# Performance work log

Hardware: AMD Instinct MI355X
Metric: run time of the kernel (lower is better)

## Reference

```python
import jax, jax.numpy as jnp
import numpy as np


def _pool_mat(N, pn):
    # F.interpolate(mode='area') == adaptive_avg_pool1d: output i averages
    # input indices [floor(i*N/pn), ceil((i+1)*N/pn))
    W = np.zeros((pn, N), dtype=np.float32)
    for i in range(pn):
        s = (i * N) // pn
        e = -((-(i + 1) * N) // pn)  # ceil((i+1)*N/pn)
        W[i, s:e] = 1.0 / (e - s)
    return W


def _up_mat(pn, N):
    # F.interpolate(mode='linear', align_corners=False) from length pn to N
    W = np.zeros((N, pn), dtype=np.float32)
    scale = pn / N
    for j in range(N):
        pos = max((j + 0.5) * scale - 0.5, 0.0)
        i0 = min(int(np.floor(pos)), pn - 1)
        i1 = min(i0 + 1, pn - 1)
        frac = pos - i0
        W[j, i0] += 1.0 - frac
        W[j, i1] += frac
    return W


def setup_inputs() -> dict:
    key = jax.random.key(0)
    k1, k2 = jax.random.split(key)
    B, N, C, K = 512, 16, 256, 8192
    f = jax.random.normal(k1, (B, N, C), dtype=jnp.float32)
    # original init: uniform(-1/K, 1/K)
    emb = jax.random.uniform(k2, (K, C), dtype=jnp.float32, minval=-1.0 / K, maxval=1.0 / K)
    return {"f": f, "emb": emb}


def reference(f, emb):
    B, N, C = f.shape
    fT = jnp.transpose(f, (0, 2, 1))            # [B, C, N]
    f_ng = jax.lax.stop_gradient(fT)
    emb_ng = jax.lax.stop_gradient(emb)
    e_sq = jnp.sum(emb_ng * emb_ng, axis=1)     # [K]
    f_rest = f_ng
    f_hat = jnp.zeros_like(f_ng)
    commit = jnp.float32(0.0)
    qlat = jnp.float32(0.0)
    for pn in range(1, N + 1):
        rest_bcn = jax.lax.stop_gradient(f_rest)
        if pn < N:
            Wp = jnp.asarray(_pool_mat(N, pn))             # [pn, N]
            rest = jnp.einsum('pn,bcn->bpc', Wp, rest_bcn).reshape(-1, C)
        else:
            rest = jnp.transpose(rest_bcn, (0, 2, 1)).reshape(-1, C)
        # squared euclidean distances [B*pn, K]
        d = jnp.sum(rest * rest, axis=1, keepdims=True) + e_sq - 2.0 * (rest @ emb_ng.T)
        idx = jnp.argmin(d, axis=1).reshape(B, pn)
        h = jnp.transpose(emb[idx], (0, 2, 1))             # [B, C, pn]
        if pn < N:
            Wu = jnp.asarray(_up_mat(pn, N))               # [N, pn]
            h = jnp.einsum('np,bcp->bcn', Wu, h)
        f_hat = f_hat + h
        f_rest = f_rest - h
        commit = commit + 0.25 * jnp.mean((jax.lax.stop_gradient(f_hat) - fT) ** 2)
        qlat = qlat + jnp.mean((f_hat - f_ng) ** 2)
    commit = commit / N
    qlat = qlat / N
    # straight-through estimator
    f_hat_out = jax.lax.stop_gradient(f_hat) - f_ng + fT
    return jnp.transpose(f_hat_out, (0, 2, 1)), commit, qlat
```

## Files before the change

### kernel.cpp

```cpp
#include <hip/hip_runtime.h>
#include <math.h>

#define BB 512
#define NN 16
#define CC 256
#define KK 8192
#define BNC (BB*NN*CC)

typedef unsigned short u16;
typedef __attribute__((ext_vector_type(8))) short bf16x8;
typedef __attribute__((ext_vector_type(4))) float f32x4;

__device__ __forceinline__ u16 f2bf(float x) {
    unsigned u = __float_as_uint(x);
    unsigned r = (u + 0x7fffu + ((u >> 16) & 1u)) >> 16;
    return (u16)r;
}

__device__ __forceinline__ void gl2lds16(const void* g, void* l) {
    __builtin_amdgcn_global_load_lds(
        (const __attribute__((address_space(1))) void*)g,
        (__attribute__((address_space(3))) void*)l,
        16, 0, 0);
}

__device__ __forceinline__ void gl2lds4(const void* g, void* l) {
    __builtin_amdgcn_global_load_lds(
        (const __attribute__((address_space(1))) void*)g,
        (__attribute__((address_space(3))) void*)l,
        4, 0, 0);
}

__global__ void esq_kernel(const float* __restrict__ emb, float* __restrict__ e_sq) {
    int gid  = blockIdx.x * blockDim.x + threadIdx.x;
    int wave = gid >> 6;
    int lane = gid & 63;
    const float4 v = *(const float4*)(emb + (size_t)wave * CC + lane * 4);
    float s = v.x*v.x + v.y*v.y + v.z*v.z + v.w*v.w;
    #pragma unroll
    for (int m = 32; m >= 1; m >>= 1) s += __shfl_xor(s, m, 64);
    if (lane == 0) e_sq[wave] = 0.5f * s;
}

__global__ void cvt_emb_kernel(const float* __restrict__ emb, u16* __restrict__ out) {
    int gid = blockIdx.x * blockDim.x + threadIdx.x;
    float4 v = ((const float4*)emb)[gid];
    ushort4 o;
    o.x = f2bf(-v.x); o.y = f2bf(-v.y); o.z = f2bf(-v.z); o.w = f2bf(-v.w);
    ((ushort4*)out)[gid] = o;
}

__global__ void init_pool_kernel(const float* __restrict__ f,
                                 u16* __restrict__ rest_bf) {
    int b = blockIdx.x;
    int c = threadIdx.x;
    const float* base = f + (size_t)b * NN * CC + c;
    float acc = 0.f;
    #pragma unroll
    for (int n = 0; n < NN; ++n) acc += base[(size_t)n * CC];
    rest_bf[(size_t)b * CC + c] = f2bf(acc * (1.0f / 16.0f));
}

__device__ __forceinline__ unsigned long long shfl_xor_u64(unsigned long long v, int m) {
    unsigned lo = (unsigned)v, hi = (unsigned)(v >> 32);
    lo = __shfl_xor(lo, m, 64);
    hi = __shfl_xor(hi, m, 64);
    return ((unsigned long long)hi << 32) | lo;
}

__global__ __launch_bounds__(256, 2) void dist_mfma_kernel(
        const u16* __restrict__ A, const u16* __restrict__ Bm,
        const float* __restrict__ e_sq,
        unsigned long long* __restrict__ packed, int cpb) {
    __shared__ __align__(16) u16 sC[32768];
    __shared__ __align__(16) float sE[512];
    const int tid = threadIdx.x;
    const int w = tid >> 6, l = tid & 63;
    const int r0 = blockIdx.x * 64;
    const int c0 = blockIdx.y * cpb;
    const int ncb = cpb >> 8;
    const int tmax = ncb * 8 - 1;
    const int arow = l & 15;
    const int aq   = l >> 4;

    bf16x8 bf[4][8];
    {
        const u16* fb = A + (((size_t)(r0 + arow)) << 8) + aq * 8;
        #pragma unroll
        for (int j = 0; j < 4; ++j)
            #pragma unroll
            for (int kc = 0; kc < 8; ++kc)
                bf[j][kc] = *(const bf16x8*)(fb + (j << 12) + (kc << 5));
    }

    const int loff = ((l >> 2) << 8) + ((l & 3) << 3);
    const u16* Pb = Bm + (((size_t)(c0 + w * 64)) << 8) + loff;
    char* ldsc = (char*)sC + (w << 14);
    const float* ebuf = sE + (w << 7);

    #define STAGEC(t_, buf_) { \
        const int tt_ = ((t_) > tmax) ? tmax : (t_); \
        const u16* s_ = Pb + (((size_t)(tt_ >> 3)) << 16) + ((tt_ & 7) << 5); \
        char* d_ = ldsc + ((buf_) << 12); \
        gl2lds16(s_,          d_); \
        gl2lds16(s_ + 4096,   d_ + 1024); \
        gl2lds16(s_ + 8192,   d_ + 2048); \
        gl2lds16(s_ + 12288,  d_ + 3072); }

    #define STAGEE(cb_) { \
        const int cc_ = ((cb_) >= ncb) ? (ncb - 1) : (cb_); \
        gl2lds4(e_sq + c0 + cc_ * 256 + w * 64 + l, \
                (char*)sE + ((((w << 1) | ((cb_) & 1))) << 8)); }

    STAGEE(0)
    STAGEC(0, 0) STAGEC(1, 1) STAGEC(2, 2)

    float bestd[4];
    int   bestk[4];
    #pragma unroll
    for (int j = 0; j < 4; ++j) { bestd[j] = 1e30f; bestk[j] = 0; }

    for (int cb = 0; cb < ncb; ++cb) {
        f32x4 acc[4][4];
        const int tb = cb * 8;
        #pragma unroll
        for (int kc = 0; kc < 8; ++kc) {
            if (kc >= 1 && kc <= 3) {
                asm volatile("s_waitcnt vmcnt(9)" ::: "memory");
            } else {
                asm volatile("s_waitcnt vmcnt(8)" ::: "memory");
            }
            if (kc == 0) {
                f32x4 eqv[4];
                #pragma unroll
                for (int i = 0; i < 4; ++i)
                    eqv[i] = *(const f32x4*)(ebuf + ((cb & 1) << 6) + i * 16 + (aq << 2));
                #pragma unroll
                for (int i = 0; i < 4; ++i)
                    #pragma unroll
                    for (int j = 0; j < 4; ++j) acc[i][j] = eqv[i];
            }
            const int t = tb + kc;
            bf16x8 cf[4];
            const u16* cbp = (const u16*)(ldsc + ((t & 3) << 12));
            #pragma unroll
            for (int i = 0; i < 4; ++i)
                cf[i] = *(const bf16x8*)(cbp + ((i * 16 + arow) << 5) + (aq << 3));
            STAGEC(t + 3, (t + 3) & 3)
            if (kc == 0) STAGEE(cb + 1)
            #pragma unroll
            for (int i = 0; i < 4; ++i)
                #pragma unroll
                for (int j = 0; j < 4; ++j)
                    acc[i][j] = __builtin_amdgcn_mfma_f32_16x16x32_bf16(
                                    cf[i], bf[j][kc], acc[i][j], 0, 0, 0);
        }

        #pragma unroll
        for (int i = 0; i < 4; ++i)
            #pragma unroll
            for (int r = 0; r < 4; ++r) {
                const int k = c0 + cb * 256 + w * 64 + i * 16 + (aq << 2) + r;
                #pragma unroll
                for (int j = 0; j < 4; ++j) {
                    const float d = acc[i][j][r];
                    if (d < bestd[j]) { bestd[j] = d; bestk[j] = k; }
                }
            }
    }
    #undef STAGEC
    #undef STAGEE

    #pragma unroll
    for (int j = 0; j < 4; ++j) {
        unsigned u = __float_as_uint(bestd[j]);
        u = (u & 0x80000000u) ? ~u : (u | 0x80000000u);
        unsigned long long p = ((unsigned long long)u << 32) | (unsigned)bestk[j];
        unsigned long long o = shfl_xor_u64(p, 16);
        if (o < p) p = o;
        o = shfl_xor_u64(p, 32);
        if (o < p) p = o;
        if (aq == 0)
            atomicMin(&packed[r0 + j * 16 + arow], p);
    }
}

__global__ void update_pool_kernel(const float* __restrict__ f,
                                   const float* __restrict__ emb,
                                   const unsigned long long* __restrict__ packed,
                                   float* __restrict__ f_rest,
                                   float* __restrict__ f_hat,
                                   float* __restrict__ slots,
                                   u16* __restrict__ rest_bf, int pn) {
    int b = blockIdx.x;
    int c = threadIdx.x;
    __shared__ int sk[NN];
    __shared__ float red[4];
    if (threadIdx.x < pn)
        sk[threadIdx.x] = (int)(unsigned)(packed[b * pn + threadIdx.x] & 0xffffffffull);
    __syncthreads();

    float fr[NN];
    float acc_sq = 0.f;
    #pragma unroll
    for (int n = 0; n < NN; ++n) {
        double pos = (n + 0.5) * ((double)pn / 16.0) - 0.5;
        if (pos < 0.0) pos = 0.0;
        int i0 = (int)floor(pos);
        if (i0 > pn - 1) i0 = pn - 1;
        int i1 = i0 + 1;
        if (i1 > pn - 1) i1 = pn - 1;
        double frac = pos - (double)i0;
        float w1 = (float)frac;
        float w0 = (float)(1.0 - frac);
        float h = w0 * emb[(size_t)sk[i0] * CC + c] + w1 * emb[(size_t)sk[i1] * CC + c];
        size_t off = ((size_t)b * NN + n) * CC + c;
        float fh = f_hat[off] + h;
        f_hat[off] = fh;
        float fre = f_rest[off] - h;
        f_rest[off] = fre;
        fr[n] = fre;
        float diff = fh - f[off];
        acc_sq += diff * diff;
    }

    int wv = threadIdx.x >> 6, ln = threadIdx.x & 63;
    #pragma unroll
    for (int m = 32; m >= 1; m >>= 1) acc_sq += __shfl_xor(acc_sq, m, 64);
    if (ln == 0) red[wv] = acc_sq;

    int pn2 = pn + 1;
    if (pn < NN) {
        for (int p = 0; p < pn2; ++p) {
            int s = (p * NN) / pn2;
            int e = ((p + 1) * NN + pn2 - 1) / pn2;
            float v = 0.f;
            for (int n = s; n < e; ++n) v += fr[n];
            v *= 1.0f / (float)(e - s);
            rest_bf[((size_t)(b * pn2 + p)) * CC + c] = f2bf(v);
        }
    }
    __syncthreads();
    if (threadIdx.x == 0)
        atomicAdd(&slots[b & 255], (red[0] + red[1]) + (red[2] + red[3]));
}

__global__ void final_kernel(const float* __restrict__ slots, float* __restrict__ out_scalars) {
    float v = slots[threadIdx.x];
    #pragma unroll
    for (int m = 32; m >= 1; m >>= 1) v += __shfl_xor(v, m, 64);
    __shared__ float red[4];
    int wv = threadIdx.x >> 6, ln = threadIdx.x & 63;
    if (ln == 0) red[wv] = v;
    __syncthreads();
    if (threadIdx.x == 0) {
        float S = (red[0] + red[1]) + (red[2] + red[3]);
        float qlat = S / (float)BNC / (float)NN;
        out_scalars[0] = 0.25f * qlat;
        out_scalars[1] = qlat;
    }
}

extern "C" void kernel_launch(void* const* d_in, const int* in_sizes, int n_in,
                              void* d_out, int out_size, void* d_ws, size_t ws_size,
                              hipStream_t stream) {
    (void)in_sizes; (void)n_in; (void)out_size; (void)ws_size;
    const float* f   = (const float*)d_in[0];
    const float* emb = (const float*)d_in[1];
    float* out = (float*)d_out;

    float* ws      = (float*)d_ws;
    float* f_rest  = ws;
    float* r2_pad  = f_rest + BNC;
    float* e_sq    = r2_pad + BB * NN;
    float* slots   = e_sq + KK;
    unsigned long long* packed_all = (unsigned long long*)(slots + 256);
    u16* rest_bf = (u16*)(packed_all + (size_t)BB * 136);
    u16* emb_bf  = rest_bf + (size_t)BB * NN * CC;

    float* f_hat = out;

    hipMemsetAsync(out, 0, (size_t)BNC * sizeof(float), stream);
    hipMemcpyAsync(f_rest, f, (size_t)BNC * sizeof(float), hipMemcpyDeviceToDevice, stream);
    hipMemsetAsync(slots, 0, 256 * sizeof(float), stream);
    hipMemsetAsync(packed_all, 0xFF, (size_t)BB * 136 * sizeof(unsigned long long), stream);
    esq_kernel<<<KK / 4, 256, 0, stream>>>(emb, e_sq);
    cvt_emb_kernel<<<KK * CC / 4 / 256, 256, 0, stream>>>(emb, emb_bf);
    init_pool_kernel<<<BB, 256, 0, stream>>>(f, rest_bf);

    static const int splits_tab[17] = {0,32,32,16,16,8,8,8,8,4,4,4,4,4,4,4,4};

    for (int pn = 1; pn <= NN; ++pn) {
        unsigned long long* packed = packed_all + (size_t)BB * (pn * (pn - 1) / 2);
        int splits = splits_tab[pn];
        int cpb = KK / splits;
        dim3 grid(BB * pn / 64, splits);
        dist_mfma_kernel<<<grid, 256, 0, stream>>>(rest_bf, emb_bf, e_sq, packed, cpb);
        update_pool_kernel<<<BB, 256, 0, stream>>>(f, emb, packed, f_rest, f_hat,
                                                   slots, rest_bf, pn);
    }
    final_kernel<<<1, 256, 0, stream>>>(slots, out + BNC);
}
```

Before: 772.0 us.

## Share codebook tiles across waves with 64-row-per-wave blocking in distance kernel

Restructures the distance MFMA kernel so each block covers 256 rows (64 per wave) and all waves share one codebook tile staged into LDS per step, instead of each wave streaming its own codebook slice. This cuts per-block global/LDS codebook traffic relative to compute. It adds an XOR swizzle to avoid LDS bank conflicts, preloads all e_sq values, and raises wave priority around MFMAs. It requires a workgroup barrier every k-step and retunes the K-split table to keep enough blocks.

Result: slower. 787.9 us (+2.1%).

```diff
diff --git a/kernel.cpp b/kernel.cpp
--- a/kernel.cpp
+++ b/kernel.cpp
@@ -76,16 +76,16 @@
     __shared__ __align__(16) float sE[512];
     const int tid = threadIdx.x;
     const int w = tid >> 6, l = tid & 63;
-    const int r0 = blockIdx.x * 64;
+    const int r0 = blockIdx.x * 256;
     const int c0 = blockIdx.y * cpb;
-    const int ncb = cpb >> 8;
-    const int tmax = ncb * 8 - 1;
+    const int nch = cpb >> 3;
+    const int ncb2 = cpb >> 6;
     const int arow = l & 15;
     const int aq   = l >> 4;
 
     bf16x8 bf[4][8];
     {
-        const u16* fb = A + (((size_t)(r0 + arow)) << 8) + aq * 8;
+        const u16* fb = A + (((size_t)(r0 + w * 64 + arow)) << 8) + aq * 8;
         #pragma unroll
         for (int j = 0; j < 4; ++j)
             #pragma unroll
@@ -93,74 +93,63 @@
                 bf[j][kc] = *(const bf16x8*)(fb + (j << 12) + (kc << 5));
     }
 
-    const int loff = ((l >> 2) << 8) + ((l & 3) << 3);
-    const u16* Pb = Bm + (((size_t)(c0 + w * 64)) << 8) + loff;
-    char* ldsc = (char*)sC + (w << 14);
-    const float* ebuf = sE + (w << 7);
-
-    #define STAGEC(t_, buf_) { \
-        const int tt_ = ((t_) > tmax) ? tmax : (t_); \
-        const u16* s_ = Pb + (((size_t)(tt_ >> 3)) << 16) + ((tt_ & 7) << 5); \
-        char* d_ = ldsc + ((buf_) << 12); \
-        gl2lds16(s_,          d_); \
-        gl2lds16(s_ + 4096,   d_ + 1024); \
-        gl2lds16(s_ + 8192,   d_ + 2048); \
-        gl2lds16(s_ + 12288,  d_ + 3072); }
-
-    #define STAGEE(cb_) { \
-        const int cc_ = ((cb_) >= ncb) ? (ncb - 1) : (cb_); \
-        gl2lds4(e_sq + c0 + cc_ * 256 + w * 64 + l, \
-                (char*)sE + ((((w << 1) | ((cb_) & 1))) << 8)); }
-
-    STAGEE(0)
-    STAGEC(0, 0) STAGEC(1, 1) STAGEC(2, 2)
-
+    for (int n = tid; n < cpb; n += 256)
+        gl2lds4(e_sq + c0 + n, (char*)sE + (size_t)(n - l) * 4);
+
+    const int crel = w * 16 + (l >> 2);
+    const int g = (l & 3) ^ ((l >> 3) & 3);
+    const u16* Pb = Bm + (((size_t)(c0 + crel)) << 8) + g * 8;
+
+    #define STAGEC(t_) { \
+        int tt_ = (t_); if (tt_ >= nch) tt_ = nch - 1; \
+        const u16* s_ = Pb + (((size_t)(tt_ >> 3)) << 14) + ((tt_ & 7) << 5); \
+        gl2lds16(s_, (char*)sC + (((t_) & 3) << 12) + (w << 10)); }
+
+    STAGEC(0) STAGEC(1) STAGEC(2)
+
+    const int gx = aq ^ ((arow >> 1) & 3);
     float bestd[4];
     int   bestk[4];
     #pragma unroll
     for (int j = 0; j < 4; ++j) { bestd[j] = 1e30f; bestk[j] = 0; }
 
-    for (int cb = 0; cb < ncb; ++cb) {
+    for (int cb = 0; cb < ncb2; ++cb) {
         f32x4 acc[4][4];
-        const int tb = cb * 8;
         #pragma unroll
         for (int kc = 0; kc < 8; ++kc) {
-            if (kc >= 1 && kc <= 3) {
-                asm volatile("s_waitcnt vmcnt(9)" ::: "memory");
-            } else {
-                asm volatile("s_waitcnt vmcnt(8)" ::: "memory");
+            const int t = cb * 8 + kc;
+            asm volatile("s_waitcnt vmcnt(2)" ::: "memory");
+            __builtin_amdgcn_s_barrier();
+            STAGEC(t + 3)
+            if (kc == 0) {
+                #pragma unroll
+                for (int i = 0; i < 4; ++i) {
+                    f32x4 ev = *(const f32x4*)(sE + cb * 64 + i * 16 + (aq << 2));
+                    #pragma unroll
+                    for (int j = 0; j < 4; ++j) acc[i][j] = ev;
+                }
             }
-            if (kc == 0) {
-                f32x4 eqv[4];
-                #pragma unroll
-                for (int i = 0; i < 4; ++i)
-                    eqv[i] = *(const f32x4*)(ebuf + ((cb & 1) << 6) + i * 16 + (aq << 2));
-                #pragma unroll
-                for (int i = 0; i < 4; ++i)
-                    #pragma unroll
-                    for (int j = 0; j < 4; ++j) acc[i][j] = eqv[i];
-            }
-            const int t = tb + kc;
             bf16x8 cf[4];
-            const u16* cbp = (const u16*)(ldsc + ((t & 3) << 12));
+            const u16* cbp = sC + ((t & 3) << 11);
             #pragma unroll
             for (int i = 0; i < 4; ++i)
-                cf[i] = *(const bf16x8*)(cbp + ((i * 16 + arow) << 5) + (aq << 3));
-            STAGEC(t + 3, (t + 3) & 3)
-            if (kc == 0) STAGEE(cb + 1)
+                cf[i] = *(const bf16x8*)(cbp + ((i * 16 + arow) << 5) + (gx << 3));
+            __builtin_amdgcn_s_setprio(1);
             #pragma unroll
             for (int i = 0; i < 4; ++i)
                 #pragma unroll
                 for (int j = 0; j < 4; ++j)
                     acc[i][j] = __builtin_amdgcn_mfma_f32_16x16x32_bf16(
                                     cf[i], bf[j][kc], acc[i][j], 0, 0, 0);
+            __builtin_amdgcn_s_setprio(0);
+            asm volatile("s_waitcnt lgkmcnt(0)" ::: "memory");
         }
 
         #pragma unroll
         for (int i = 0; i < 4; ++i)
             #pragma unroll
             for (int r = 0; r < 4; ++r) {
-                const int k = c0 + cb * 256 + w * 64 + i * 16 + (aq << 2) + r;
+                const int k = c0 + cb * 64 + i * 16 + (aq << 2) + r;
                 #pragma unroll
                 for (int j = 0; j < 4; ++j) {
                     const float d = acc[i][j][r];
@@ -169,7 +158,6 @@
             }
     }
     #undef STAGEC
-    #undef STAGEE
 
     #pragma unroll
     for (int j = 0; j < 4; ++j) {
@@ -181,7 +169,7 @@
         o = shfl_xor_u64(p, 32);
         if (o < p) p = o;
         if (aq == 0)
-            atomicMin(&packed[r0 + j * 16 + arow], p);
+            atomicMin(&packed[r0 + w * 64 + j * 16 + arow], p);
     }
 }
 
@@ -288,13 +276,14 @@
     cvt_emb_kernel<<<KK * CC / 4 / 256, 256, 0, stream>>>(emb, emb_bf);
     init_pool_kernel<<<BB, 256, 0, stream>>>(f, rest_bf);
 
-    static const int splits_tab[17] = {0,32,32,16,16,8,8,8,8,4,4,4,4,4,4,4,4};
+    static const int splits_tab[17] =
+        {0,128,64,64,32,32,32,32,16,16,16,16,16,16,16,16,16};
 
     for (int pn = 1; pn <= NN; ++pn) {
         unsigned long long* packed = packed_all + (size_t)BB * (pn * (pn - 1) / 2);
         int splits = splits_tab[pn];
         int cpb = KK / splits;
-        dim3 grid(BB * pn / 64, splits);
+        dim3 grid(BB * pn / 256, splits);
         dist_mfma_kernel<<<grid, 256, 0, stream>>>(rest_bf, emb_bf, e_sq, packed, cpb);
         update_pool_kernel<<<BB, 256, 0, stream>>>(f, emb, packed, f_rest, f_hat,
                                                    slots, rest_bf, pn);
```
